# Performance work log

Measured on AMD Instinct MI355X. Metric: run time of the kernel, lower is better.

## Reference

```python
import jax, jax.numpy as jnp
import numpy as np

N_NODES = 100000
N_EDGES = 3200000
NUM_FEATURES = 256
NUM_CLASSES = 1000


def gcn_conv(x, edge_index, W, b):
    # PyG GCNConv: h = XW; add self-loops; out = D^{-1/2} (A+I) D^{-1/2} h + b
    n = x.shape[0]
    h = x @ W  # [N, out]
    loop = jnp.arange(n)
    src = jnp.concatenate([edge_index[0], loop])
    dst = jnp.concatenate([edge_index[1], loop])
    ones = jnp.ones(src.shape[0], dtype=x.dtype)
    deg = jax.ops.segment_sum(ones, dst, num_segments=n)  # in-degree incl. self-loop
    dinv = jax.lax.rsqrt(deg)  # deg >= 1 because of self-loops
    norm = dinv[src] * dinv[dst]  # [E+N]
    out = jax.ops.segment_sum(h[src] * norm[:, None], dst, num_segments=n)
    return out + b


def setup_inputs() -> dict:
    key = jax.random.key(0)
    ks = jax.random.split(key, 12)
    x = jax.random.normal(ks[0], (N_NODES, NUM_FEATURES), dtype=jnp.float32)
    edge_index = jax.random.randint(ks[1], (2, N_EDGES), 0, N_NODES, dtype=jnp.int64)
    def glorot(k, shape):
        fan_in, fan_out = shape[0], shape[-1]
        lim = np.sqrt(6.0 / (fan_in + fan_out)).astype(np.float32)
        return jax.random.uniform(k, shape, jnp.float32, -lim, lim)
    W1 = glorot(ks[2], (NUM_FEATURES, 16)); b1 = jnp.zeros((16,), jnp.float32)
    W2 = glorot(ks[3], (16, 32));           b2 = jnp.zeros((32,), jnp.float32)
    conv_w = jax.random.normal(ks[4], (64, 32, 1, 3), jnp.float32) * 0.05  # OIHW
    conv_b = jnp.zeros((64,), jnp.float32)
    fc_w = jax.random.normal(ks[5], (NUM_CLASSES, 64), jnp.float32) * 0.05
    fc_b = jnp.zeros((NUM_CLASSES,), jnp.float32)
    return {"x": x, "edge_index": edge_index, "W1": W1, "b1": b1,
            "W2": W2, "b2": b2, "conv_w": conv_w, "conv_b": conv_b,
            "fc_w": fc_w, "fc_b": fc_b}


def reference(x, edge_index, W1, b1, W2, b2, conv_w, conv_b, fc_w, fc_b):
    h = jax.nn.relu(gcn_conv(x, edge_index, W1, b1))   # [N,16]
    h = gcn_conv(h, edge_index, W2, b2)                 # [N,32]
    # x.unsqueeze(0).transpose(1,2) -> [1, 32, N]; run Conv2d((1,3), pad (0,1))
    # as NCHW with H=1: [1, 32, 1, N]
    img = h.T[None, :, None, :]                         # [1,32,1,N]
    y = jax.lax.conv_general_dilated(
        img, conv_w, window_strides=(1, 1), padding=((0, 0), (1, 1)),
        dimension_numbers=("NCHW", "OIHW", "NCHW"))
    y = y + conv_b[None, :, None, None]                 # [1,64,1,N]
    # adaptive_max_pool2d to (1,1) == global max over spatial dims
    pooled = jnp.max(y, axis=(2, 3))                    # [1,64]
    return pooled @ fc_w.T + fc_b                       # [1,num_classes]
```

## Files before the change

### kernel.cpp

```cpp
#include <hip/hip_runtime.h>
#include <hip/hip_bf16.h>
#include <hip/hip_fp16.h>

#define NN 100000
#define NE 3200000
#define FIN 256
#define F1 16
#define F2 32
#define CO 64
#define NC 1000
#define NBLK 391
#define GBLK 1563
#define NPART 8
#define NGRP 32
#define CAPG 16384
#define PSZ 12500
#define BK 20
#define SRCMASK 0x1FFFFu

#define OFF_DINV 0
#define OFF_CUR  100352
#define OFF_DEG  200704
#define OFF_ECOL 301056
#define OFF_MISC 3501056
#define OFF_EPART 3502080
#define OFF_HIST  7696384
#define OFF_H1S   3502080
#define OFF_H2S   4302080
#define OFF_OUT2H 5902080

__device__ __forceinline__ unsigned enc_f(float f) {
    unsigned u = __float_as_uint(f);
    return (u & 0x80000000u) ? ~u : (u | 0x80000000u);
}
__device__ __forceinline__ float dec_f(unsigned u) {
    return (u & 0x80000000u) ? __uint_as_float(u & 0x7fffffffu) : __uint_as_float(~u);
}

__global__ void k_init(unsigned* __restrict__ pcur, unsigned* __restrict__ pool) {
    int t = threadIdx.x;
    pcur[t] = (unsigned)t * CAPG;
    if (t < 64) pool[t] = 0u;
}

__global__ __launch_bounds__(256) void k_bucket(const int* __restrict__ ei,
                                                unsigned* __restrict__ pcur,
                                                unsigned* __restrict__ epart) {
    __shared__ unsigned wcnt[4][8];
    __shared__ unsigned woff[4][8];
    int t = threadIdx.x, lane = t & 63, w = t >> 6;
    int g = blockIdx.x & (NGRP - 1);
    int base = blockIdx.x * (256 * BK) + t;
    int dst[BK], src[BK];
    #pragma unroll
    for (int k = 0; k < BK; ++k) {
        dst[k] = ei[NE + base + k * 256];
        src[k] = ei[base + k * 256];
    }
    unsigned long long lt = (lane == 63) ? 0x7fffffffffffffffull
                                         : ((1ull << lane) - 1ull);
    unsigned cnt = 0;
    #pragma unroll
    for (int k = 0; k < BK; ++k) {
        int bin = (unsigned)dst[k] / PSZ;
        #pragma unroll
        for (int b = 0; b < 8; ++b) {
            unsigned long long m = __ballot(bin == b);
            if (lane == b) cnt += (unsigned)__popcll(m);
        }
    }
    if (lane < 8) wcnt[w][lane] = cnt;
    __syncthreads();
    if (t < 8) {
        unsigned c0 = wcnt[0][t], c1 = wcnt[1][t], c2 = wcnt[2][t], c3 = wcnt[3][t];
        unsigned b = atomicAdd(&pcur[t * NGRP + g], c0 + c1 + c2 + c3);
        woff[0][t] = b;
        woff[1][t] = b + c0;
        woff[2][t] = b + c0 + c1;
        woff[3][t] = b + c0 + c1 + c2;
    }
    __syncthreads();
    unsigned run = (lane < 8) ? woff[w][lane] : 0u;
    #pragma unroll
    for (int k = 0; k < BK; ++k) {
        int bin = (unsigned)dst[k] / PSZ;
        unsigned long long mym = 0;
        unsigned myrun = 0;
        #pragma unroll
        for (int b = 0; b < 8; ++b) {
            unsigned long long m = __ballot(bin == b);
            unsigned r = __shfl(run, b);
            if (bin == b) { mym = m; myrun = r; }
            if (lane == b) run += (unsigned)__popcll(m);
        }
        unsigned pos = myrun + (unsigned)__popcll(mym & lt);
        epart[pos] = ((unsigned)(dst[k] - bin * PSZ) << 17) | (unsigned)src[k];
    }
}

__global__ __launch_bounds__(256) void k_hist(const unsigned* __restrict__ pcur,
                                              const unsigned* __restrict__ epart,
                                              unsigned* __restrict__ hist) {
    __shared__ unsigned lh[PSZ];
    int p = blockIdx.x & 7;
    int g = blockIdx.x >> 3;
    int ci = p * NGRP + g;
    int t = threadIdx.x;
    for (int i = t; i < PSZ; i += 256) lh[i] = 0;
    __syncthreads();
    unsigned s = (unsigned)ci * CAPG;
    unsigned e = pcur[ci];
    for (unsigned j = s + t; j < e; j += 256)
        atomicAdd(&lh[epart[j] >> 17], 1u);
    __syncthreads();
    unsigned* hrow = hist + (unsigned)ci * PSZ;
    for (int i = t; i < PSZ; i += 256) hrow[i] = lh[i];
}

__global__ __launch_bounds__(256) void k_colscan(unsigned* __restrict__ hist,
                                                 unsigned* __restrict__ deg,
                                                 unsigned* __restrict__ bsum) {
    __shared__ unsigned W[4];
    int t = threadIdx.x;
    int gid = blockIdx.x * 256 + t;
    unsigned run = 0;
    if (gid < NN) {
        int p = gid / PSZ, i = gid % PSZ;
        #pragma unroll
        for (int c = 0; c < NGRP; ++c) {
            unsigned idx = (unsigned)(p * NGRP + c) * PSZ + i;
            unsigned v = hist[idx];
            hist[idx] = run;
            run += v;
        }
        deg[gid] = run;
    }
    unsigned d = (gid < NN) ? run : 0u;
    #pragma unroll
    for (int off = 1; off < 64; off <<= 1) d += __shfl_xor(d, off);
    if ((t & 63) == 0) W[t >> 6] = d;
    __syncthreads();
    if (t == 0) bsum[blockIdx.x] = W[0] + W[1] + W[2] + W[3];
}

__global__ __launch_bounds__(512) void k_bscan(unsigned* __restrict__ bsum) {
    __shared__ unsigned S[512];
    int t = threadIdx.x;
    unsigned v = (t < NBLK) ? bsum[t] : 0u;
    S[t] = v;
    __syncthreads();
    for (int off = 1; off < 512; off <<= 1) {
        unsigned u = (t >= off) ? S[t - off] : 0u;
        __syncthreads();
        S[t] += u;
        __syncthreads();
    }
    if (t < NBLK) bsum[t] = S[t] - v;
}

__global__ void k_cscan(const unsigned* __restrict__ deg, const unsigned* __restrict__ bsum,
                        unsigned* __restrict__ cursor, float* __restrict__ dinv) {
    __shared__ unsigned S[256];
    int t = threadIdx.x;
    int i = blockIdx.x * 256 + t;
    unsigned d = (i < NN) ? deg[i] : 0u;
    S[t] = d;
    __syncthreads();
    for (int off = 1; off < 256; off <<= 1) {
        unsigned u = (t >= off) ? S[t - off] : 0u;
        __syncthreads();
        S[t] += u;
        __syncthreads();
    }
    if (i < NN) {
        cursor[i] = bsum[blockIdx.x] + S[t];
        dinv[i] = rsqrtf((float)(d + 1u));
    }
}

__global__ __launch_bounds__(256) void k_place(const unsigned* __restrict__ pcur,
                                               const unsigned* __restrict__ epart,
                                               const unsigned* __restrict__ hist,
                                               const unsigned* __restrict__ cursor,
                                               int* __restrict__ ecol) {
    __shared__ unsigned lcur[PSZ];
    int p = blockIdx.x & 7;
    int g = blockIdx.x >> 3;
    int ci = p * NGRP + g;
    int t = threadIdx.x;
    int pb = p * PSZ;
    const unsigned* hrow = hist + (unsigned)ci * PSZ;
    for (int i = t; i < PSZ; i += 256) {
        int gi = pb + i;
        unsigned rowstart = gi ? cursor[gi - 1] : 0u;
        lcur[i] = rowstart + hrow[i];
    }
    __syncthreads();
    unsigned s = (unsigned)ci * CAPG;
    unsigned e = pcur[ci];
    for (unsigned j = s + t; j < e; j += 256) {
        unsigned v = epart[j];
        unsigned pos = atomicAdd(&lcur[v >> 17], 1u);
        ecol[pos] = (int)(v & SRCMASK);
    }
}

__device__ __forceinline__ void fma16g(float xk, const float* __restrict__ w,
                                       float* __restrict__ acc) {
    #pragma unroll
    for (int o = 0; o < 16; ++o) acc[o] += xk * w[o];
}

__global__ __launch_bounds__(64) void k_gemm1(const float* __restrict__ X,
                                              const float* __restrict__ W1,
                                              const float* __restrict__ dinv,
                                              __half2* __restrict__ h1h) {
    int row = blockIdx.x * 64 + threadIdx.x;
    if (row >= NN) return;
    const float4* xr = (const float4*)(X + (size_t)row * FIN);
    float acc[16] = {};
    #pragma unroll 1
    for (int c = 0; c < 8; ++c) {
        float4 xq[8];
        #pragma unroll
        for (int i = 0; i < 8; ++i) xq[i] = xr[c * 8 + i];
        const float* xf = (const float*)xq;
        #pragma unroll
        for (int kk = 0; kk < 32; ++kk)
            fma16g(xf[kk], W1 + (c * 32 + kk) * 16, acc);
    }
    float dv = dinv[row];
    union { __half2 h[8]; uint4 u[2]; } pk;
    #pragma unroll
    for (int o = 0; o < 8; ++o)
        pk.h[o] = __floats2half2_rn(acc[2 * o] * dv, acc[2 * o + 1] * dv);
    uint4* dst = (uint4*)(h1h + (size_t)row * 8);
    dst[0] = pk.u[0];
    dst[1] = pk.u[1];
}

__global__ __launch_bounds__(256) void k_gathm(const unsigned* __restrict__ cursor,
                                               const int* __restrict__ ecol,
                                               const float* __restrict__ dinv,
                                               const float* __restrict__ b1,
                                               const float* __restrict__ W2,
                                               const __half2* __restrict__ h1h,
                                               __half2* __restrict__ h2h) {
    __shared__ float Ws[512];
    __shared__ float B1[16];
    int tid = threadIdx.x;
    Ws[tid] = W2[tid];
    Ws[tid + 256] = W2[tid + 256];
    if (tid < 16) B1[tid] = b1[tid];
    __syncthreads();
    int lane = tid & 63;
    int grp = lane >> 3, f2 = lane & 7;
    int gb = lane & 56;
    int node = blockIdx.x * 32 + (tid >> 6) * 8 + grp;
    unsigned s = node ? cursor[node - 1] : 0u;
    unsigned e = cursor[node];
    float2 acc = __half22float2(h1h[(size_t)node * 8 + f2]);
    for (unsigned j = s; j < e; j += 8) {
        unsigned jj = j + (unsigned)f2;
        int myc = ecol[jj < e ? jj : j];
        int cq[8];
        #pragma unroll
        for (int q = 0; q < 8; ++q) cq[q] = __shfl(myc, gb + q);
        float2 a[8];
        #pragma unroll
        for (int q = 0; q < 8; ++q)
            a[q] = __half22float2(h1h[(size_t)cq[q] * 8 + f2]);
        #pragma unroll
        for (int q = 0; q < 8; ++q) {
            float m = (j + q < e) ? 1.f : 0.f;
            acc.x += m * a[q].x;
            acc.y += m * a[q].y;
        }
    }
    float dv = dinv[node];
    float r0 = fmaxf(acc.x * dv + B1[2 * f2], 0.f);
    float r1 = fmaxf(acc.y * dv + B1[2 * f2 + 1], 0.f);
    float rv[16];
    #pragma unroll
    for (int q = 0; q < 8; ++q) {
        rv[2 * q]     = __shfl(r0, gb + q);
        rv[2 * q + 1] = __shfl(r1, gb + q);
    }
    float o0x = 0.f, o0y = 0.f, o1x = 0.f, o1y = 0.f;
    #pragma unroll
    for (int q = 0; q < 16; ++q) {
        float r = rv[q];
        o0x += r * Ws[q * 32 + 2 * f2];
        o0y += r * Ws[q * 32 + 2 * f2 + 1];
        o1x += r * Ws[q * 32 + 2 * f2 + 16];
        o1y += r * Ws[q * 32 + 2 * f2 + 17];
    }
    h2h[(size_t)node * 16 + f2]     = __floats2half2_rn(o0x * dv, o0y * dv);
    h2h[(size_t)node * 16 + f2 + 8] = __floats2half2_rn(o1x * dv, o1y * dv);
}

__global__ __launch_bounds__(256) void k_gath2(const unsigned* __restrict__ cursor,
                                               const int* __restrict__ ecol,
                                               const float* __restrict__ dinv,
                                               const float* __restrict__ b2,
                                               const __half2* __restrict__ h2h,
                                               __half2* __restrict__ out2h) {
    int tid = threadIdx.x;
    int lane = tid & 63;
    int grp = lane >> 4, f2 = lane & 15;
    int gb = lane & 48;
    int node = blockIdx.x * 16 + (tid >> 6) * 4 + grp;
    unsigned s = node ? cursor[node - 1] : 0u;
    unsigned e = cursor[node];
    float2 acc = __half22float2(h2h[(size_t)node * 16 + f2]);
    for (unsigned j = s; j < e; j += 16) {
        unsigned jj = j + (unsigned)f2;
        int myc = ecol[jj < e ? jj : j];
        int cq[16];
        #pragma unroll
        for (int q = 0; q < 16; ++q) cq[q] = __shfl(myc, gb + q);
        float2 a[16];
        #pragma unroll
        for (int q = 0; q < 16; ++q)
            a[q] = __half22float2(h2h[(size_t)cq[q] * 16 + f2]);
        #pragma unroll
        for (int q = 0; q < 16; ++q) {
            float m = (j + q < e) ? 1.f : 0.f;
            acc.x += m * a[q].x;
            acc.y += m * a[q].y;
        }
    }
    float dv = dinv[node];
    float2 b = ((const float2*)b2)[f2];
    out2h[(size_t)node * 16 + f2] =
        __floats2half2_rn(acc.x * dv + b.x, acc.y * dv + b.y);
}

#define NPB 256
__global__ __launch_bounds__(256) void k_conv(const __half2* __restrict__ h2f,
                                              const float* __restrict__ cw,
                                              unsigned* __restrict__ pool) {
    __shared__ float Hs[NPB + 2][33];
    __shared__ float Wt[3 * 32 * 64];
    __shared__ float4 Ms[4][16];
    int tid = threadIdx.x;
    int base = blockIdx.x * NPB;
    for (int idx = tid; idx < 6144; idx += 256) {
        int o = idx / 96, r = idx % 96, ci = r / 3, k = r % 3;
        Wt[(k * 32 + ci) * 64 + o] = cw[idx];
    }
    for (int idx = tid; idx < (NPB + 2) * 4; idx += 256) {
        int j = idx >> 2, qt = idx & 3;
        int g = base + j - 1;
        if (g >= 0 && g < NN) {
            uint4 v = *(const uint4*)(h2f + (size_t)g * 16 + qt * 4);
            const __half2* hp = (const __half2*)&v;
            #pragma unroll
            for (int q = 0; q < 4; ++q) {
                float2 f = __half22float2(hp[q]);
                Hs[j][qt * 8 + 2 * q]     = f.x;
                Hs[j][qt * 8 + 2 * q + 1] = f.y;
            }
        } else {
            #pragma unroll
            for (int q = 0; q < 8; ++q) Hs[j][qt * 8 + q] = 0.f;
        }
    }
    __syncthreads();

    int o4 = (tid & 15) * 4;
    int ng = tid >> 4;
    float4 acc[16] = {};
    for (int ci = 0; ci < 32; ++ci) {
        float h[18];
        #pragma unroll
        for (int j = 0; j < 18; ++j) h[j] = Hs[ng * 16 + j][ci];
        #pragma unroll
        for (int k = 0; k < 3; ++k) {
            float4 w = *(const float4*)&Wt[(k * 32 + ci) * 64 + o4];
            #pragma unroll
            for (int i = 0; i < 16; ++i) {
                float hv = h[i + k];
                acc[i].x += hv * w.x;
                acc[i].y += hv * w.y;
                acc[i].z += hv * w.z;
                acc[i].w += hv * w.w;
            }
        }
    }
    const float NI = -3.0e38f;
    float4 m4 = make_float4(NI, NI, NI, NI);
    #pragma unroll
    for (int i = 0; i < 16; ++i) {
        if (base + ng * 16 + i < NN) {
            m4.x = fmaxf(m4.x, acc[i].x);
            m4.y = fmaxf(m4.y, acc[i].y);
            m4.z = fmaxf(m4.z, acc[i].z);
            m4.w = fmaxf(m4.w, acc[i].w);
        }
    }
    #pragma unroll
    for (int off = 16; off <= 32; off <<= 1) {
        m4.x = fmaxf(m4.x, __shfl_xor(m4.x, off));
        m4.y = fmaxf(m4.y, __shfl_xor(m4.y, off));
        m4.z = fmaxf(m4.z, __shfl_xor(m4.z, off));
        m4.w = fmaxf(m4.w, __shfl_xor(m4.w, off));
    }
    int lane = tid & 63, wv = tid >> 6;
    if (lane < 16) Ms[wv][lane] = m4;
    __syncthreads();
    if (tid < 16) {
        float4 a = Ms[0][tid], b = Ms[1][tid], c = Ms[2][tid], d = Ms[3][tid];
        a.x = fmaxf(fmaxf(a.x, b.x), fmaxf(c.x, d.x));
        a.y = fmaxf(fmaxf(a.y, b.y), fmaxf(c.y, d.y));
        a.z = fmaxf(fmaxf(a.z, b.z), fmaxf(c.z, d.z));
        a.w = fmaxf(fmaxf(a.w, b.w), fmaxf(c.w, d.w));
        int o = tid * 4;
        atomicMax(&pool[o + 0], enc_f(a.x));
        atomicMax(&pool[o + 1], enc_f(a.y));
        atomicMax(&pool[o + 2], enc_f(a.z));
        atomicMax(&pool[o + 3], enc_f(a.w));
    }
}

__global__ void k_fc(const unsigned* __restrict__ pool, const float* __restrict__ cb,
                     const float* __restrict__ fw, const float* __restrict__ fb,
                     float* __restrict__ out) {
    __shared__ float P[64];
    int tid = threadIdx.x;
    if (tid < 64) P[tid] = dec_f(pool[tid]) + cb[tid];
    __syncthreads();
    int j = blockIdx.x * 256 + tid;
    if (j >= NC) return;
    float s = fb[j];
    const float4* wr = (const float4*)(fw + (size_t)j * CO);
    #pragma unroll
    for (int c = 0; c < 16; ++c) {
        float4 w = wr[c];
        s += P[c * 4 + 0] * w.x + P[c * 4 + 1] * w.y +
             P[c * 4 + 2] * w.z + P[c * 4 + 3] * w.w;
    }
    out[j] = s;
}

extern "C" void kernel_launch(void* const* d_in, const int* in_sizes, int n_in,
                              void* d_out, int out_size, void* d_ws, size_t ws_size,
                              hipStream_t stream) {
    const float* x  = (const float*)d_in[0];
    const int*   ei = (const int*)d_in[1];
    const float* W1 = (const float*)d_in[2];
    const float* b1 = (const float*)d_in[3];
    const float* W2 = (const float*)d_in[4];
    const float* b2 = (const float*)d_in[5];
    const float* cw = (const float*)d_in[6];
    const float* cb = (const float*)d_in[7];
    const float* fw = (const float*)d_in[8];
    const float* fb = (const float*)d_in[9];

    float* ws = (float*)d_ws;
    float*    dinv   = ws + OFF_DINV;
    unsigned* cursor = (unsigned*)(ws + OFF_CUR);
    unsigned* deg    = (unsigned*)(ws + OFF_DEG);
    int*      ecol   = (int*)(ws + OFF_ECOL);
    unsigned* pcur   = (unsigned*)(ws + OFF_MISC);
    unsigned* pool   = pcur + 256;
    unsigned* bsum   = pcur + 320;
    unsigned* epart  = (unsigned*)(ws + OFF_EPART);
    unsigned* hist   = (unsigned*)(ws + OFF_HIST);
    __half2*  h1h    = (__half2*)(ws + OFF_H1S);
    __half2*  h2h    = (__half2*)(ws + OFF_H2S);
    __half2*  out2h  = (__half2*)(ws + OFF_OUT2H);

    k_init   <<<1, 256, 0, stream>>>(pcur, pool);
    k_bucket <<<NE / (256 * BK), 256, 0, stream>>>(ei, pcur, epart);
    k_hist   <<<NPART * NGRP, 256, 0, stream>>>(pcur, epart, hist);
    k_colscan<<<NBLK, 256, 0, stream>>>(hist, deg, bsum);
    k_bscan  <<<1, 512, 0, stream>>>(bsum);
    k_cscan  <<<NBLK, 256, 0, stream>>>(deg, bsum, cursor, dinv);
    k_place  <<<NPART * NGRP, 256, 0, stream>>>(pcur, epart, hist, cursor, ecol);
    k_gemm1  <<<GBLK, 64, 0, stream>>>(x, W1, dinv, h1h);
    k_gathm  <<<NN / 32, 256, 0, stream>>>(cursor, ecol, dinv, b1, W2, h1h, h2h);
    k_gath2  <<<NN / 16, 256, 0, stream>>>(cursor, ecol, dinv, b2, h2h, out2h);
    k_conv   <<<(NN + NPB - 1) / NPB, 256, 0, stream>>>(out2h, cw, pool);
    k_fc     <<<4, 256, 0, stream>>>(pool, cb, fw, fb, (float*)d_out);
}
```

Measured before the change: 241.9 us.

## Tile first-layer GEMM through shared memory with coalesced X loads

Rewrites the X·W1 kernel so that each 256-thread block stages 64 rows × 32 columns of X into shared memory with coalesced float4 loads and transposes them. W1 is held in shared memory, and each thread computes 4 output columns for one row. Previously each thread streamed its own 1 KB row, which gave strided, uncoalesced access and left only 64 threads per block. The cost is extra shared-memory traffic and two barriers per k-tile.

```diff
diff --git a/kernel.cpp b/kernel.cpp
--- a/kernel.cpp
+++ b/kernel.cpp
@@ -205,38 +205,55 @@
     }
 }
 
-__device__ __forceinline__ void fma16g(float xk, const float* __restrict__ w,
-                                       float* __restrict__ acc) {
-    #pragma unroll
-    for (int o = 0; o < 16; ++o) acc[o] += xk * w[o];
-}
-
-__global__ __launch_bounds__(64) void k_gemm1(const float* __restrict__ X,
-                                              const float* __restrict__ W1,
-                                              const float* __restrict__ dinv,
-                                              __half2* __restrict__ h1h) {
-    int row = blockIdx.x * 64 + threadIdx.x;
-    if (row >= NN) return;
-    const float4* xr = (const float4*)(X + (size_t)row * FIN);
-    float acc[16] = {};
-    #pragma unroll 1
-    for (int c = 0; c < 8; ++c) {
-        float4 xq[8];
-        #pragma unroll
-        for (int i = 0; i < 8; ++i) xq[i] = xr[c * 8 + i];
-        const float* xf = (const float*)xq;
-        #pragma unroll
-        for (int kk = 0; kk < 32; ++kk)
-            fma16g(xf[kk], W1 + (c * 32 + kk) * 16, acc);
-    }
-    float dv = dinv[row];
-    union { __half2 h[8]; uint4 u[2]; } pk;
-    #pragma unroll
-    for (int o = 0; o < 8; ++o)
-        pk.h[o] = __floats2half2_rn(acc[2 * o] * dv, acc[2 * o + 1] * dv);
-    uint4* dst = (uint4*)(h1h + (size_t)row * 8);
-    dst[0] = pk.u[0];
-    dst[1] = pk.u[1];
+__global__ __launch_bounds__(256) void k_gemm1(const float* __restrict__ X,
+                                               const float* __restrict__ W1,
+                                               const float* __restrict__ dinv,
+                                               __half2* __restrict__ h1h) {
+    __shared__ float Xs[32][65];
+    __shared__ float4 Ws[1024];
+    int tid = threadIdx.x;
+    const float4* W14 = (const float4*)W1;
+    for (int i = tid; i < 1024; i += 256) Ws[i] = W14[i];
+
+    int rowbase = blockIdx.x * 64;
+    int q  = tid >> 2;
+    int cg = tid & 3;
+    float4 acc = make_float4(0.f, 0.f, 0.f, 0.f);
+
+    for (int kt = 0; kt < 8; ++kt) {
+        __syncthreads();
+        #pragma unroll
+        for (int it = 0; it < 2; ++it) {
+            int fl = tid + it * 256;
+            int rl = fl >> 3;
+            int c4 = (fl & 7) << 2;
+            int gr = rowbase + rl;
+            float4 v = make_float4(0.f, 0.f, 0.f, 0.f);
+            if (gr < NN) v = *(const float4*)(X + (size_t)gr * FIN + kt * 32 + c4);
+            Xs[c4 + 0][rl] = v.x;
+            Xs[c4 + 1][rl] = v.y;
+            Xs[c4 + 2][rl] = v.z;
+            Xs[c4 + 3][rl] = v.w;
+        }
+        __syncthreads();
+        #pragma unroll
+        for (int kk = 0; kk < 32; ++kk) {
+            float4 w4 = Ws[(kt * 32 + kk) * 4 + cg];
+            float xv = Xs[kk][q];
+            acc.x += xv * w4.x;
+            acc.y += xv * w4.y;
+            acc.z += xv * w4.z;
+            acc.w += xv * w4.w;
+        }
+    }
+    int r = rowbase + q;
+    if (r < NN) {
+        float dv = dinv[r];
+        union { __half2 h[2]; uint2 u; } pk;
+        pk.h[0] = __floats2half2_rn(acc.x * dv, acc.y * dv);
+        pk.h[1] = __floats2half2_rn(acc.z * dv, acc.w * dv);
+        *(uint2*)(h1h + (size_t)r * 8 + cg * 2) = pk.u;
+    }
 }
 
 __global__ __launch_bounds__(256) void k_gathm(const unsigned* __restrict__ cursor,
@@ -478,7 +495,7 @@
     k_bscan  <<<1, 512, 0, stream>>>(bsum);
     k_cscan  <<<NBLK, 256, 0, stream>>>(deg, bsum, cursor, dinv);
     k_place  <<<NPART * NGRP, 256, 0, stream>>>(pcur, epart, hist, cursor, ecol);
-    k_gemm1  <<<GBLK, 64, 0, stream>>>(x, W1, dinv, h1h);
+    k_gemm1  <<<GBLK, 256, 0, stream>>>(x, W1, dinv, h1h);
     k_gathm  <<<NN / 32, 256, 0, stream>>>(cursor, ecol, dinv, b1, W2, h1h, h2h);
     k_gath2  <<<NN / 16, 256, 0, stream>>>(cursor, ecol, dinv, b2, h2h, out2h);
     k_conv   <<<(NN + NPB - 1) / NPB, 256, 0, stream>>>(out2h, cw, pool);
```

After: 246.7 us. About the same (+2.0%).
